# Kernel tuning notes

Measured on AMD Instinct MI355X. Metric: run time of the kernel, lower is better.

Reference implementation:

```python
import jax, jax.numpy as jnp
import numpy as np

BASE_DIM = 256
FIBER_DIM = 64
BATCH = 4096
PATH_LEN = 512


def setup_inputs() -> dict:
    key = jax.random.key(0)
    k1, k2, k3 = jax.random.split(key, 3)
    fiber_state = jax.random.normal(k1, (BATCH, FIBER_DIM), dtype=jnp.float32)
    base_path = jax.random.uniform(k2, (BATCH, PATH_LEN), dtype=jnp.float32)
    # torch init is identity expanded over base_dim; add small noise so the
    # learned parameter is non-trivial while repeated products stay bounded.
    connection = (jnp.eye(FIBER_DIM, dtype=jnp.float32)[None, :, :]
                  + 0.01 * jax.random.normal(k3, (BASE_DIM, FIBER_DIM, FIBER_DIM), dtype=jnp.float32))
    return {"fiber_state": fiber_state, "base_path": base_path, "connection": connection}


def reference(fiber_state, base_path, connection):
    # fiber_state: [B, f]; base_path: [B, L]; connection: [base_dim, f, f]
    base_dim = connection.shape[0]
    xs = base_path[:, :-1].T  # [L-1, B], one path step per scan iteration

    def step(t, bp):
        # per-step index derived from path values, normalized by batch max (clamped at 1)
        mx = jnp.maximum(jnp.max(bp), 1.0)
        idx = jnp.clip((bp * base_dim / mx).astype(jnp.int32), 0, base_dim - 1)  # [B]
        mats = connection[idx]  # [B, f, f] gather
        t = jnp.einsum('bi,bij->bj', t, mats)  # row-vector times matrix (torch bmm of [B,1,f]x[B,f,f])
        return t, None

    transported, _ = jax.lax.scan(step, fiber_state, xs)
    return transported
```

## Files before the change

kernel.cpp:

```cpp
#include <hip/hip_runtime.h>
#include <stdint.h>

#define BATCH 4096
#define PLEN  512
#define NSTEP 511
#define FD    64


__global__ void k_init_colmax(unsigned int* cm) {
    int t = threadIdx.x;
    if (t < PLEN) cm[t] = 0x3f800000u;
}

__global__ void k_colmax(const float* __restrict__ bp, unsigned int* __restrict__ cm) {
    __shared__ float red[256];
    int tx = threadIdx.x & 63;
    int ty = threadIdx.x >> 6;
    int t  = blockIdx.x * 64 + tx;
    int b0 = blockIdx.y * 256 + ty * 64;
    const float* p = bp + (size_t)b0 * PLEN + t;
    float m = 0.0f;
    #pragma unroll 4
    for (int r = 0; r < 64; ++r) {
        m = fmaxf(m, p[(size_t)r * PLEN]);
    }
    red[threadIdx.x] = m;
    __syncthreads();
    if (ty == 0) {
        m = fmaxf(fmaxf(red[tx], red[64 + tx]), fmaxf(red[128 + tx], red[192 + tx]));
        atomicMax((int*)&cm[t], __float_as_int(m));
    }
}

__global__ void k_idx(const float* __restrict__ bp, const unsigned int* __restrict__ cm,
                      uint8_t* __restrict__ idx) {
    int gid = blockIdx.x * blockDim.x + threadIdx.x;
    int t = gid & (PLEN - 1);
    uint8_t k = 0;
    if (t < NSTEP) {
        float mx = __uint_as_float(cm[t]);
        float v  = bp[gid];
        float q  = (v * 256.0f) / mx;
        int ik = (int)q;
        ik = ik < 0 ? 0 : (ik > 255 ? 255 : ik);
        k = (uint8_t)ik;
    }
    idx[gid] = k;
}

__device__ __forceinline__ unsigned short f2h(float x) {
    _Float16 h = (_Float16)x;
    return __builtin_bit_cast(unsigned short, h);
}

__global__ void k_pack(const float* __restrict__ conn, uint4* __restrict__ ph) {
    int gid = blockIdx.x * blockDim.x + threadIdx.x;
    int j = gid & 63;
    int m = (gid >> 6) & 7;
    int k = gid >> 9;
    const float* M = conn + ((size_t)k << 12);
    unsigned int w[4];
    #pragma unroll
    for (int d = 0; d < 4; ++d) {
        int i0 = 8 * m + 2 * d, i1 = i0 + 1;
        float x0 = M[i0 * 64 + j] - (i0 == j ? 1.0f : 0.0f);
        float x1 = M[i1 * 64 + j] - (i1 == j ? 1.0f : 0.0f);
        w[d] = (unsigned)f2h(x0) | ((unsigned)f2h(x1) << 16);
    }
    ph[gid] = make_uint4(w[0], w[1], w[2], w[3]);
}

#define MIXLO(P, BC, PK) \
    asm("v_fma_mix_f32 %0, %1, %2, %0 op_sel_hi:[0,1,0]" : "+v"(P) : "v"(BC), "v"(PK))
#define MIXHI(P, BC, PK) \
    asm("v_fma_mix_f32 %0, %1, %2, %0 op_sel:[0,1,0] op_sel_hi:[0,1,0]" : "+v"(P) : "v"(BC), "v"(PK))

__device__ __forceinline__ float step16(float acc, const uint4 buf[8], float* sa, int lane) {
    sa[lane] = acc;
    asm volatile("s_waitcnt lgkmcnt(0)" ::: "memory");
    float p0 = acc, p1 = 0.f, p2 = 0.f, p3 = 0.f;
    const float4* sv = (const float4*)sa;
    #pragma unroll
    for (int q = 0; q < 8; ++q) {
        uint4 B = buf[q];
        float4 b0 = sv[2 * q];
        float4 b1 = sv[2 * q + 1];
        MIXLO(p0, b0.x, B.x); MIXHI(p1, b0.y, B.x);
        MIXLO(p2, b0.z, B.y); MIXHI(p3, b0.w, B.y);
        MIXLO(p0, b1.x, B.z); MIXHI(p1, b1.y, B.z);
        MIXLO(p2, b1.z, B.w); MIXHI(p3, b1.w, B.w);
    }
    return (p0 + p1) + (p2 + p3);
}

__global__ void __launch_bounds__(256) k_chain(
    const float* __restrict__ fiber, const uint8_t* __restrict__ idx,
    const uint4* __restrict__ ph, float* __restrict__ out)
{
    __shared__ uint64_t sidx64[4][64];
    __shared__ float4 sacc4[4][16];
    int wid  = threadIdx.x >> 6;
    int lane = threadIdx.x & 63;
    int b = blockIdx.x * 4 + wid;

    sidx64[wid][lane] = ((const uint64_t*)(idx + (size_t)b * PLEN))[lane];
    __syncthreads();
    const uint8_t* si = (const uint8_t*)sidx64[wid];
    float* sa = (float*)&sacc4[wid][0];

    float acc = fiber[b * FD + lane];

    uint4 bufA[8], bufB[8];

    int k0 = __builtin_amdgcn_readfirstlane((int)si[0]);
    {
        const uint4* M = ph + ((size_t)k0 << 9);
        #pragma unroll
        for (int m = 0; m < 8; ++m) bufA[m] = M[m * 64 + lane];
    }
    int kn = (int)si[1];

    for (int i = 0; i < 255; ++i) {
        int kb = __builtin_amdgcn_readfirstlane(kn);
        {
            const uint4* M = ph + ((size_t)kb << 9);
            #pragma unroll
            for (int m = 0; m < 8; ++m) bufB[m] = M[m * 64 + lane];
        }
        int kn2 = (int)si[2 * i + 2];
        acc = step16(acc, bufA, sa, lane);
        int ka = __builtin_amdgcn_readfirstlane(kn2);
        {
            const uint4* M = ph + ((size_t)ka << 9);
            #pragma unroll
            for (int m = 0; m < 8; ++m) bufA[m] = M[m * 64 + lane];
        }
        kn = (int)si[2 * i + 3];
        acc = step16(acc, bufB, sa, lane);
    }
    acc = step16(acc, bufA, sa, lane);

    out[b * FD + lane] = acc;
}

extern "C" void kernel_launch(void* const* d_in, const int* in_sizes, int n_in,
                              void* d_out, int out_size, void* d_ws, size_t ws_size,
                              hipStream_t stream) {
    const float* fiber = (const float*)d_in[0];
    const float* bp    = (const float*)d_in[1];
    const float* conn  = (const float*)d_in[2];
    float* out = (float*)d_out;

    unsigned int* cm = (unsigned int*)d_ws;
    uint8_t* idx = (uint8_t*)d_ws + 2048;
    uint4* ph = (uint4*)((uint8_t*)d_ws + 2048 + (size_t)BATCH * PLEN);

    hipLaunchKernelGGL(k_init_colmax, dim3(1), dim3(512), 0, stream, cm);
    hipLaunchKernelGGL(k_colmax, dim3(8, 16), dim3(256), 0, stream, bp, cm);
    hipLaunchKernelGGL(k_idx, dim3((BATCH * PLEN) / 256), dim3(256), 0, stream, bp, cm, idx);
    hipLaunchKernelGGL(k_pack, dim3(512), dim3(256), 0, stream, conn, ph);
    hipLaunchKernelGGL(k_chain, dim3(BATCH / 4), dim3(256), 0, stream, fiber, idx, ph, out);
}
```

Measured before the change: 553.0 us.

## Triple-buffer matrix prefetch with inline-asm loads and fuse idx/pack kernels

Replaces the double-buffered matrix loads in the chain kernel with a three-deep rotation. Each stage issues eight dwordx4 loads through inline asm and waits with explicit vmcnt counts, so two matrices stay in flight while one is consumed. The index and pack kernels are merged into a single launch to remove one kernel launch, and launch bounds now ask for higher occupancy. The third buffer raises register pressure, and the hand-written waitcnt accounting is fragile.

```diff
diff --git a/kernel.cpp b/kernel.cpp
--- a/kernel.cpp
+++ b/kernel.cpp
@@ -32,42 +32,44 @@
     }
 }
 
-__global__ void k_idx(const float* __restrict__ bp, const unsigned int* __restrict__ cm,
-                      uint8_t* __restrict__ idx) {
-    int gid = blockIdx.x * blockDim.x + threadIdx.x;
-    int t = gid & (PLEN - 1);
-    uint8_t k = 0;
-    if (t < NSTEP) {
-        float mx = __uint_as_float(cm[t]);
-        float v  = bp[gid];
-        float q  = (v * 256.0f) / mx;
-        int ik = (int)q;
-        ik = ik < 0 ? 0 : (ik > 255 ? 255 : ik);
-        k = (uint8_t)ik;
-    }
-    idx[gid] = k;
-}
-
 __device__ __forceinline__ unsigned short f2h(float x) {
     _Float16 h = (_Float16)x;
     return __builtin_bit_cast(unsigned short, h);
 }
 
-__global__ void k_pack(const float* __restrict__ conn, uint4* __restrict__ ph) {
-    int gid = blockIdx.x * blockDim.x + threadIdx.x;
-    int j = gid & 63;
-    int m = (gid >> 6) & 7;
-    int k = gid >> 9;
-    const float* M = conn + ((size_t)k << 12);
-    unsigned int w[4];
-    #pragma unroll
-    for (int d = 0; d < 4; ++d) {
-        int i0 = 8 * m + 2 * d, i1 = i0 + 1;
-        float x0 = M[i0 * 64 + j] - (i0 == j ? 1.0f : 0.0f);
-        float x1 = M[i1 * 64 + j] - (i1 == j ? 1.0f : 0.0f);
-        w[d] = (unsigned)f2h(x0) | ((unsigned)f2h(x1) << 16);
+__global__ void k_idx_pack(const float* __restrict__ bp, const unsigned int* __restrict__ cm,
+                           uint8_t* __restrict__ idx, const float* __restrict__ conn,
+                           uint4* __restrict__ ph) {
+    int bid = blockIdx.x;
+    if (bid < (BATCH * PLEN) / 256) {
+        int gid = bid * 256 + threadIdx.x;
+        int t = gid & (PLEN - 1);
+        uint8_t k = 0;
+        if (t < NSTEP) {
+            float mx = __uint_as_float(cm[t]);
+            float v  = bp[gid];
+            float q  = (v * 256.0f) / mx;
+            int ik = (int)q;
+            ik = ik < 0 ? 0 : (ik > 255 ? 255 : ik);
+            k = (uint8_t)ik;
+        }
+        idx[gid] = k;
+    } else {
+        int gid = (bid - (BATCH * PLEN) / 256) * 256 + threadIdx.x;
+        int j = gid & 63;
+        int m = (gid >> 6) & 7;
+        int k = gid >> 9;
+        const float* M = conn + ((size_t)k << 12);
+        unsigned int w[4];
+        #pragma unroll
+        for (int d = 0; d < 4; ++d) {
+            int i0 = 8 * m + 2 * d, i1 = i0 + 1;
+            float x0 = M[i0 * 64 + j] - (i0 == j ? 1.0f : 0.0f);
+            float x1 = M[i1 * 64 + j] - (i1 == j ? 1.0f : 0.0f);
+            w[d] = (unsigned)f2h(x0) | ((unsigned)f2h(x1) << 16);
+        }
+        ph[gid] = make_uint4(w[0], w[1], w[2], w[3]);
     }
-    ph[gid] = make_uint4(w[0], w[1], w[2], w[3]);
 }
 
 #define MIXLO(P, BC, PK) \
@@ -93,7 +95,28 @@
     return (p0 + p1) + (p2 + p3);
 }
 
-__global__ void __launch_bounds__(256) k_chain(
+#define ISSUE8(B, KS) do {                                                     \
+    const char* _b = ph_c + ((size_t)(unsigned)(KS) << 13);                    \
+    asm volatile(                                                              \
+        "global_load_dwordx4 %0, %8, %9\n\t"                                   \
+        "global_load_dwordx4 %1, %8, %9 offset:1024\n\t"                       \
+        "global_load_dwordx4 %2, %8, %9 offset:2048\n\t"                       \
+        "global_load_dwordx4 %3, %8, %9 offset:3072\n\t"                       \
+        "global_load_dwordx4 %4, %10, %9\n\t"                                  \
+        "global_load_dwordx4 %5, %10, %9 offset:1024\n\t"                      \
+        "global_load_dwordx4 %6, %10, %9 offset:2048\n\t"                      \
+        "global_load_dwordx4 %7, %10, %9 offset:3072"                          \
+        : "=&v"(B[0]), "=&v"(B[1]), "=&v"(B[2]), "=&v"(B[3]),                  \
+          "=&v"(B[4]), "=&v"(B[5]), "=&v"(B[6]), "=&v"(B[7])                   \
+        : "v"(voff0), "s"(_b), "v"(voff1));                                    \
+} while (0)
+
+#define WAITC(N) do {                                                          \
+    asm volatile("s_waitcnt vmcnt(" #N ")" ::: "memory");                      \
+    __builtin_amdgcn_sched_barrier(0);                                         \
+} while (0)
+
+__global__ void __launch_bounds__(256, 4) k_chain(
     const float* __restrict__ fiber, const uint8_t* __restrict__ idx,
     const uint4* __restrict__ ph, float* __restrict__ out)
 {
@@ -107,38 +130,43 @@
     __syncthreads();
     const uint8_t* si = (const uint8_t*)sidx64[wid];
     float* sa = (float*)&sacc4[wid][0];
+    const char* ph_c = (const char*)ph;
+
+    unsigned voff0 = (unsigned)lane * 16u;
+    unsigned voff1 = voff0 + 4096u;
 
     float acc = fiber[b * FD + lane];
+    asm volatile("s_waitcnt vmcnt(0)" : "+v"(acc));
 
-    uint4 bufA[8], bufB[8];
+    uint4 b0_[8], b1_[8], b2_[8];
 
-    int k0 = __builtin_amdgcn_readfirstlane((int)si[0]);
-    {
-        const uint4* M = ph + ((size_t)k0 << 9);
-        #pragma unroll
-        for (int m = 0; m < 8; ++m) bufA[m] = M[m * 64 + lane];
+    ISSUE8(b0_, __builtin_amdgcn_readfirstlane((int)si[0]));
+    ISSUE8(b1_, __builtin_amdgcn_readfirstlane((int)si[1]));
+
+    int s = 0;
+    #pragma unroll 1
+    for (int it = 0; it < 169; ++it) {
+        ISSUE8(b2_, __builtin_amdgcn_readfirstlane((int)si[s + 2]));
+        WAITC(16);
+        acc = step16(acc, b0_, sa, lane);
+        ISSUE8(b0_, __builtin_amdgcn_readfirstlane((int)si[s + 3]));
+        WAITC(16);
+        acc = step16(acc, b1_, sa, lane);
+        ISSUE8(b1_, __builtin_amdgcn_readfirstlane((int)si[s + 4]));
+        WAITC(16);
+        acc = step16(acc, b2_, sa, lane);
+        s += 3;
     }
-    int kn = (int)si[1];
-
-    for (int i = 0; i < 255; ++i) {
-        int kb = __builtin_amdgcn_readfirstlane(kn);
-        {
-            const uint4* M = ph + ((size_t)kb << 9);
-            #pragma unroll
-            for (int m = 0; m < 8; ++m) bufB[m] = M[m * 64 + lane];
-        }
-        int kn2 = (int)si[2 * i + 2];
-        acc = step16(acc, bufA, sa, lane);
-        int ka = __builtin_amdgcn_readfirstlane(kn2);
-        {
-            const uint4* M = ph + ((size_t)ka << 9);
-            #pragma unroll
-            for (int m = 0; m < 8; ++m) bufA[m] = M[m * 64 + lane];
-        }
-        kn = (int)si[2 * i + 3];
-        acc = step16(acc, bufB, sa, lane);
-    }
-    acc = step16(acc, bufA, sa, lane);
+    ISSUE8(b2_, __builtin_amdgcn_readfirstlane((int)si[509]));
+    WAITC(16);
+    acc = step16(acc, b0_, sa, lane);
+    ISSUE8(b0_, __builtin_amdgcn_readfirstlane((int)si[510]));
+    WAITC(16);
+    acc = step16(acc, b1_, sa, lane);
+    WAITC(8);
+    acc = step16(acc, b2_, sa, lane);
+    WAITC(0);
+    acc = step16(acc, b0_, sa, lane);
 
     out[b * FD + lane] = acc;
 }
@@ -157,7 +185,7 @@
 
     hipLaunchKernelGGL(k_init_colmax, dim3(1), dim3(512), 0, stream, cm);
     hipLaunchKernelGGL(k_colmax, dim3(8, 16), dim3(256), 0, stream, bp, cm);
-    hipLaunchKernelGGL(k_idx, dim3((BATCH * PLEN) / 256), dim3(256), 0, stream, bp, cm, idx);
-    hipLaunchKernelGGL(k_pack, dim3(512), dim3(256), 0, stream, conn, ph);
+    hipLaunchKernelGGL(k_idx_pack, dim3((BATCH * PLEN) / 256 + 512), dim3(256), 0, stream,
+                       bp, cm, idx, conn, ph);
     hipLaunchKernelGGL(k_chain, dim3(BATCH / 4), dim3(256), 0, stream, fiber, idx, ph, out);
 }
```

Result: slower. 573.6 us (+3.7%).
